# Kernel optimization log

Hardware: AMD Instinct MI355X
Metric: run time of the kernel (lower is better)

## Reference

```python
import jax, jax.numpy as jnp
import numpy as np

N_HEAD, D_MODEL, D_K, D_V = 8, 512, 64, 64
WINDOW, THRESH = 2, 0.5
TEMP = float(np.sqrt(D_K))
LN_EPS = 1e-5


def setup_inputs() -> dict:
    key = jax.random.key(0)
    ks = jax.random.split(key, 12)
    B, L = 4, 2048
    std_qk = np.sqrt(2.0 / (D_MODEL + D_K))
    std_v = np.sqrt(2.0 / (D_MODEL + D_V))
    return {
        "q": jax.random.normal(ks[0], (B, L, D_MODEL), jnp.float32),
        "k": jax.random.normal(ks[1], (B, L, D_MODEL), jnp.float32),
        "v": jax.random.normal(ks[2], (B, L, D_MODEL), jnp.float32),
        "w_q": jax.random.normal(ks[3], (N_HEAD * D_K, D_MODEL), jnp.float32) * std_qk,
        "b_q": jnp.zeros((N_HEAD * D_K,), jnp.float32),
        "w_k": jax.random.normal(ks[4], (N_HEAD * D_K, D_MODEL), jnp.float32) * std_qk,
        "b_k": jnp.zeros((N_HEAD * D_K,), jnp.float32),
        "w_v": jax.random.normal(ks[5], (N_HEAD * D_V, D_MODEL), jnp.float32) * std_v,
        "b_v": jnp.zeros((N_HEAD * D_V,), jnp.float32),
        "w_g": jax.random.normal(ks[6], (1, D_K), jnp.float32) * (1.0 / np.sqrt(D_K)),
        "b_g": jnp.zeros((1,), jnp.float32),
        "w_fc": jax.random.normal(ks[7], (D_MODEL, N_HEAD * D_V), jnp.float32) * (1.0 / np.sqrt(D_MODEL)),
        "b_fc": jnp.zeros((D_MODEL,), jnp.float32),
        "ln_g": jnp.ones((D_MODEL,), jnp.float32),
        "ln_b": jnp.zeros((D_MODEL,), jnp.float32),
    }


def reference(q, k, v, w_q, b_q, w_k, b_k, w_v, b_v, w_g, b_g, w_fc, b_fc, ln_g, ln_b):
    B, Lq, _ = q.shape
    Lk = k.shape[1]
    residual = q
    # project and split heads: (h, B, L, d)
    qh = (q @ w_q.T + b_q).reshape(B, Lq, N_HEAD, D_K).transpose(2, 0, 1, 3)
    kh = (k @ w_k.T + b_k).reshape(B, Lk, N_HEAD, D_K).transpose(2, 0, 1, 3)
    vh = (v @ w_v.T + b_v).reshape(B, Lk, N_HEAD, D_V).transpose(2, 0, 1, 3)

    scores = jnp.einsum('hbqd,hbkd->hbqk', qh, kh) / TEMP  # (h, B, Lq, Lk)

    # dynamic gate: tokens with sigmoid(gate) > THRESH keep full attention,
    # others are restricted to a +/-WINDOW sliding window
    gate_open = jax.nn.sigmoid(jnp.einsum('hbqd,od->hbqo', qh, w_g) + b_g)[..., 0] > THRESH
    i = jnp.arange(Lq)[:, None]
    j = jnp.arange(Lk)[None, :]
    win = jnp.abs(i - j) <= WINDOW  # (Lq, Lk)
    allowed = gate_open[..., None] | win  # (h, B, Lq, Lk)
    scores = jnp.where(allowed, scores, -jnp.inf)

    attn = jax.nn.softmax(scores, axis=-1)  # dropout is identity in eval
    out = jnp.einsum('hbqk,hbkd->hbqd', attn, vh)
    out = out.transpose(1, 2, 0, 3).reshape(B, Lq, N_HEAD * D_V)
    out = out @ w_fc.T + b_fc

    x = out + residual
    mu = jnp.mean(x, axis=-1, keepdims=True)
    var = jnp.mean((x - mu) ** 2, axis=-1, keepdims=True)
    out = (x - mu) * jax.lax.rsqrt(var + LN_EPS) * ln_g + ln_b

    return out, attn.reshape(N_HEAD * B, Lq, Lk)
```

## Files before the change

### kernel.cpp

```cpp
#include <hip/hip_runtime.h>


typedef _Float16 f16;
typedef _Float16 f16x8 __attribute__((ext_vector_type(8)));
typedef _Float16 f16x4 __attribute__((ext_vector_type(4)));
typedef float f32x4 __attribute__((ext_vector_type(4)));

#define OUT0_ELEMS (4 * 2048 * 512)

__device__ __forceinline__ f16x8 cvt8(float4 a, float4 b) {
  f16x8 r;
  r[0] = (f16)a.x; r[1] = (f16)a.y; r[2] = (f16)a.z; r[3] = (f16)a.w;
  r[4] = (f16)b.x; r[5] = (f16)b.y; r[6] = (f16)b.z; r[7] = (f16)b.w;
  return r;
}

__global__ __launch_bounds__(256) void prep_kernel(
    const float* __restrict__ w_q, const float* __restrict__ b_q,
    const float* __restrict__ w_g, const float* __restrict__ b_g,
    double* __restrict__ wge, double* __restrict__ bqg) {
  int idx = blockIdx.x * 256 + threadIdx.x;
  if (idx < 4096) {
    int h = idx >> 9, c = idx & 511;
    double acc = 0.0;
    for (int d = 0; d < 64; ++d)
      acc += (double)w_g[d] * (double)w_q[(h * 64 + d) * 512 + c];
    wge[idx] = acc;
  }
  if (idx < 8) {
    double acc = (double)b_g[0];
    for (int d = 0; d < 64; ++d)
      acc += (double)b_q[idx * 64 + d] * (double)w_g[d];
    bqg[idx] = acc;
  }
}

__global__ __launch_bounds__(256) void gate_kernel(
    const float* __restrict__ q, const double* __restrict__ wge,
    const double* __restrict__ bqg, int* __restrict__ gate) {
  int lane = threadIdx.x & 63, wid = threadIdx.x >> 6;
  int tok = blockIdx.x * 4 + wid;
  int b = tok >> 11, l = tok & 2047;
  const float* qr = q + (long)tok * 512;
  float qv[8];
#pragma unroll
  for (int j = 0; j < 8; ++j) qv[j] = qr[lane + 64 * j];
#pragma unroll
  for (int h = 0; h < 8; ++h) {
    double acc = 0.0;
#pragma unroll
    for (int j = 0; j < 8; ++j) acc += (double)qv[j] * wge[h * 512 + lane + 64 * j];
#pragma unroll
    for (int off = 1; off < 64; off <<= 1) acc += __shfl_xor(acc, off);
    double logit = acc + bqg[h];
    if (lane == 0) gate[(h * 4 + b) * 2048 + l] = (logit > 0.0) ? 1 : 0;
  }
}

__global__ __launch_bounds__(256) void compact_kernel(
    const int* __restrict__ gate, unsigned short* __restrict__ perm,
    int* __restrict__ nopen) {
  __shared__ int wsum[4];
  const int hb = blockIdx.x, t = threadIdx.x;
  const int lane = t & 63, wid = t >> 6;
  const int base = hb * 2048;
  int g[8];
  int cnt = 0;
#pragma unroll
  for (int i = 0; i < 8; ++i) { g[i] = gate[base + t * 8 + i]; cnt += g[i]; }
  int inc = cnt;
#pragma unroll
  for (int off = 1; off < 64; off <<= 1) {
    int y = __shfl_up(inc, off);
    if (lane >= off) inc += y;
  }
  if (lane == 63) wsum[wid] = inc;
  __syncthreads();
  int wbase = 0;
  for (int w = 0; w < wid; ++w) wbase += wsum[w];
  const int totOpen = wsum[0] + wsum[1] + wsum[2] + wsum[3];
  int openPos = wbase + inc - cnt;
  int closedPos = totOpen + t * 8 - openPos;
#pragma unroll
  for (int i = 0; i < 8; ++i) {
    int l = t * 8 + i;
    if (g[i]) perm[base + openPos++] = (unsigned short)l;
    else      perm[base + closedPos++] = (unsigned short)l;
  }
  if (t == 0) nopen[hb] = totOpen;
}

template <int EPI>
__global__ __launch_bounds__(256) void gemm512(
    const float* __restrict__ A, const float* __restrict__ W,
    const float* __restrict__ bias, const float* __restrict__ res,
    f16* __restrict__ out16, float* __restrict__ outf) {
  __shared__ __align__(16) f16 As[64 * 32];
  __shared__ __align__(16) f16 Ws[64 * 32];
  const int tid = threadIdx.x;
  const int lane = tid & 63, wid = tid >> 6;
  const int lo = lane & 15, hi = lane >> 4;
  const int m0 = blockIdx.x * 64, n0 = blockIdx.y * 64;
  const int wm = wid >> 1, wn = wid & 1;

  const int srow = tid >> 2, sseg = tid & 3;
  const int ssu = sseg ^ (srow & 3);
  const float* gA = A + (long)(m0 + srow) * 512 + sseg * 8;
  const float* gW = W + (long)(n0 + srow) * 512 + sseg * 8;
  f16* wA = &As[srow * 32 + ssu * 8];
  f16* wW = &Ws[srow * 32 + ssu * 8];

  const f32x4 zero4 = {0.f, 0.f, 0.f, 0.f};
  f32x4 acc[2][2] = {{zero4, zero4}, {zero4, zero4}};
  const int ra0 = wm * 32 + lo;
  const int rb0 = wn * 32 + lo;
  const int sa = hi ^ (ra0 & 3);
  const int sb = hi ^ (rb0 & 3);

  for (int kk = 0; kk < 512; kk += 32) {
    float4 a0 = *(const float4*)(gA + kk);
    float4 a1 = *(const float4*)(gA + kk + 4);
    float4 w0 = *(const float4*)(gW + kk);
    float4 w1 = *(const float4*)(gW + kk + 4);
    *(f16x8*)wA = cvt8(a0, a1);
    *(f16x8*)wW = cvt8(w0, w1);
    __syncthreads();
    f16x8 af0 = *(const f16x8*)&As[ra0 * 32 + sa * 8];
    f16x8 af1 = *(const f16x8*)&As[(ra0 + 16) * 32 + sa * 8];
    f16x8 bf0 = *(const f16x8*)&Ws[rb0 * 32 + sb * 8];
    f16x8 bf1 = *(const f16x8*)&Ws[(rb0 + 16) * 32 + sb * 8];
    acc[0][0] = __builtin_amdgcn_mfma_f32_16x16x32_f16(af0, bf0, acc[0][0], 0, 0, 0);
    acc[0][1] = __builtin_amdgcn_mfma_f32_16x16x32_f16(af0, bf1, acc[0][1], 0, 0, 0);
    acc[1][0] = __builtin_amdgcn_mfma_f32_16x16x32_f16(af1, bf0, acc[1][0], 0, 0, 0);
    acc[1][1] = __builtin_amdgcn_mfma_f32_16x16x32_f16(af1, bf1, acc[1][1], 0, 0, 0);
    __syncthreads();
  }

#pragma unroll
  for (int i = 0; i < 2; ++i)
#pragma unroll
    for (int j = 0; j < 2; ++j)
#pragma unroll
      for (int r = 0; r < 4; ++r) {
        const int m = m0 + wm * 32 + i * 16 + hi * 4 + r;
        const int n = n0 + wn * 32 + j * 16 + lo;
        float v = acc[i][j][r] + bias[n];
        if constexpr (EPI == 0) {
          const int b = m >> 11, l = m & 2047, h = n >> 6, d = n & 63;
          out16[(long)((h * 4 + b) * 2048 + l) * 64 + d] = (f16)v;
        } else if constexpr (EPI == 2) {
          const int b = m >> 11, l = m & 2047, h = n >> 6, d = n & 63;
          out16[(long)((h * 4 + b) * 64 + d) * 2048 + l] = (f16)v;
        } else {
          outf[(long)m * 512 + n] = v + res[(long)m * 512 + n];
        }
      }
}

struct Stg2 { uint4 d0, d1; };

__device__ __forceinline__ Stg2 ldK(const f16* __restrict__ g, int tid) {
  Stg2 s;
  s.d0 = *(const uint4*)(g + tid * 8);
  s.d1 = *(const uint4*)(g + 2048 + tid * 8);
  return s;
}

__device__ __forceinline__ Stg2 ldV(const f16* __restrict__ g, int tid) {
  const int row = tid >> 3, seg = tid & 7;
  const f16* p = g + (long)row * 2048 + seg * 8;
  Stg2 s;
  s.d0 = *(const uint4*)p;
  s.d1 = *(const uint4*)(p + 32 * 2048);
  return s;
}

__device__ __forceinline__ void stW(const Stg2& s, f16* lds, int tid) {
  const int row = tid >> 3, seg = tid & 7, sw = row & 7;
  *(uint4*)&lds[(row << 6) + ((seg ^ sw) << 3)] = s.d0;
  *(uint4*)&lds[((row + 32) << 6) + ((seg ^ sw) << 3)] = s.d1;
}

__global__ __launch_bounds__(256) void attn_kernel(
    const f16* __restrict__ qh, const f16* __restrict__ kh,
    const f16* __restrict__ vt, const int* __restrict__ gate,
    const unsigned short* __restrict__ perm, const int* __restrict__ nopen,
    float* __restrict__ attn, float* __restrict__ o) {
  __shared__ __align__(16) f16 Ks[2][4096];
  __shared__ __align__(16) f16 Vs[2][4096];
  __shared__ __align__(16) f16 Ps[4][1024];
  const int tid = threadIdx.x;
  const int lane = tid & 63, wid = tid >> 6;
  const int bid = blockIdx.x;

  if (bid >= 1024) {
    const int vb = bid - 1024;
    const int hb = vb >> 5, chunk = vb & 31;
    const int nop = nopen[hb];
    const int j0 = ((nop + 63) & ~63) + (chunk << 6);
    if (j0 >= 2048) return;
    unsigned short* rowIdx = (unsigned short*)&Ks[0][0];
    if (tid < 64) rowIdx[tid] = perm[hb * 2048 + j0 + tid];
    __syncthreads();
    float* abase = attn + ((long)hb * 2048 << 11);
    const f32x4 zero4 = {0.f, 0.f, 0.f, 0.f};
#pragma unroll 4
    for (int it = 0; it < 128; ++it) {
      const int c = tid + (it << 8);
      const int ri = c >> 9;
      const int col = (c & 511) << 2;
      *(f32x4*)(abase + ((long)rowIdx[ri] << 11) + col) = zero4;
    }
    __syncthreads();
    const f16* qhb = qh + (long)hb * 2048 * 64;
    const f16* khb = kh + (long)hb * 2048 * 64;
    const f16* vtb = vt + (long)hb * 64 * 2048;
    const int b = hb & 3, h = hb >> 2;
    for (int rr = 0; rr < 16; ++rr) {
      const int row = rowIdx[(wid << 4) + rr];
      const int jlo = max(row - 2, 0), jhi = min(row + 2, 2047);
      const float qv = (float)qhb[(long)row * 64 + lane];
      float p0, p1, p2, p3, p4, sum = 0.f;
#pragma unroll
      for (int jj = 0; jj < 5; ++jj) {
        const int j = jlo + jj;
        const int js = min(j, 2047);
        float prod = qv * (float)khb[(long)js * 64 + lane];
        prod += __shfl_xor(prod, 1);
        prod += __shfl_xor(prod, 2);
        prod += __shfl_xor(prod, 4);
        prod += __shfl_xor(prod, 8);
        prod += __shfl_xor(prod, 16);
        prod += __shfl_xor(prod, 32);
        const float e = (j <= jhi) ? __expf(prod * 0.125f) : 0.f;
        if (jj == 0) p0 = e; else if (jj == 1) p1 = e; else if (jj == 2) p2 = e;
        else if (jj == 3) p3 = e; else p4 = e;
        sum += e;
      }
      const float inv = 1.f / sum;
      float pv = p0;
      pv = (lane == 1) ? p1 : pv;
      pv = (lane == 2) ? p2 : pv;
      pv = (lane == 3) ? p3 : pv;
      pv = (lane == 4) ? p4 : pv;
      if (lane < 5 && (jlo + lane) <= jhi)
        abase[((long)row << 11) + jlo + lane] = pv * inv;
      float od = 0.f;
      od += p0 * (float)vtb[(long)lane * 2048 + min(jlo + 0, 2047)];
      od += p1 * (float)vtb[(long)lane * 2048 + min(jlo + 1, 2047)];
      od += p2 * (float)vtb[(long)lane * 2048 + min(jlo + 2, 2047)];
      od += p3 * (float)vtb[(long)lane * 2048 + min(jlo + 3, 2047)];
      od += p4 * (float)vtb[(long)lane * 2048 + min(jlo + 4, 2047)];
      o[(long)(b * 2048 + row) * 512 + (h << 6) + lane] = od * inv;
    }
    return;
  }

  const int lo = lane & 15, hi = lane >> 4;
  const int xcd = bid & 7, local = bid >> 3;
  const int hb = xcd * 4 + (local >> 5);
  const int q0 = (local & 31) << 6;
  const int nop = nopen[hb];
  if (q0 >= nop) return;

  const unsigned short* pm = perm + hb * 2048 + q0;
  const f16* khb = kh + (long)hb * 2048 * 64;
  const f16* vtb = vt + (long)hb * 64 * 2048;

  const int rowA = pm[(wid << 4) + lo];
  const f16* qrow = qh + (long)(hb * 2048 + rowA) * 64;
  const f16x8 aq0 = *(const f16x8*)(qrow + (hi << 3));
  const f16x8 aq1 = *(const f16x8*)(qrow + 32 + (hi << 3));

  int qi[4], gt[4];
  float psum[4];
#pragma unroll
  for (int r = 0; r < 4; ++r) {
    qi[r] = pm[(wid << 4) + (hi << 2) + r];
    gt[r] = gate[hb * 2048 + qi[r]];
    psum[r] = 0.f;
  }
  const f32x4 zero4 = {0.f, 0.f, 0.f, 0.f};

  {
    Stg2 kreg = ldK(khb, tid);
    stW(kreg, &Ks[0][0], tid);
    kreg = ldK(khb + 4096, tid);
    int cur = 0;
    for (int kt = 0; kt < 32; ++kt) {
      __syncthreads();
      if (kt < 31) {
        stW(kreg, &Ks[cur ^ 1][0], tid);
        if (kt < 30) kreg = ldK(khb + (long)(kt + 2) * 4096, tid);
      }
      const f16* Kc = &Ks[cur][0];
      f32x4 sacc[4] = {zero4, zero4, zero4, zero4};
      __builtin_amdgcn_s_setprio(1);
#pragma unroll
      for (int s = 0; s < 2; ++s) {
        const f16x8 a = s ? aq1 : aq0;
#pragma unroll
        for (int nt = 0; nt < 4; ++nt) {
          const int krow = (nt << 4) + lo;
          const f16x8 b = *(const f16x8*)&Kc[(krow << 6) + ((((s << 2) + hi) ^ (krow & 7)) << 3)];
          sacc[nt] = __builtin_amdgcn_mfma_f32_16x16x32_f16(a, b, sacc[nt], 0, 0, 0);
        }
      }
      __builtin_amdgcn_s_setprio(0);
      const int kkb = (kt << 6) + lo;
#pragma unroll
      for (int nt = 0; nt < 4; ++nt) {
        const int kk = kkb + (nt << 4);
#pragma unroll
        for (int r = 0; r < 4; ++r) {
          const bool allowed = gt[r] || ((unsigned)(kk - qi[r] + 2) <= 4u);
          psum[r] += allowed ? __expf(sacc[nt][r] * 0.125f) : 0.f;
        }
      }
      cur ^= 1;
    }
  }

  float invl[4];
#pragma unroll
  for (int r = 0; r < 4; ++r) {
    float s = psum[r];
    s += __shfl_xor(s, 1);
    s += __shfl_xor(s, 2);
    s += __shfl_xor(s, 4);
    s += __shfl_xor(s, 8);
    invl[r] = 1.f / s;
  }

  f32x4 oacc[4] = {zero4, zero4, zero4, zero4};
  f16* Pw = &Ps[wid][0];
  const int row2 = lane >> 2, qq = lane & 3;
  float* arow = attn + ((long)(hb * 2048 + pm[(wid << 4) + row2]) << 11);

  {
    Stg2 kreg = ldK(khb, tid);
    Stg2 vreg = ldV(vtb, tid);
    stW(kreg, &Ks[0][0], tid);
    stW(vreg, &Vs[0][0], tid);
    kreg = ldK(khb + 4096, tid);
    vreg = ldV(vtb + 64, tid);
    int cur = 0;
    for (int kt = 0; kt < 32; ++kt) {
      __syncthreads();
      if (kt < 31) {
        stW(kreg, &Ks[cur ^ 1][0], tid);
        stW(vreg, &Vs[cur ^ 1][0], tid);
        if (kt < 30) {
          kreg = ldK(khb + (long)(kt + 2) * 4096, tid);
          vreg = ldV(vtb + ((kt + 2) << 6), tid);
        }
      }
      const f16* Kc = &Ks[cur][0];
      const f16* Vc = &Vs[cur][0];
      f32x4 sacc[4] = {zero4, zero4, zero4, zero4};
      __builtin_amdgcn_s_setprio(1);
#pragma unroll
      for (int s = 0; s < 2; ++s) {
        const f16x8 a = s ? aq1 : aq0;
#pragma unroll
        for (int nt = 0; nt < 4; ++nt) {
          const int krow = (nt << 4) + lo;
          const f16x8 b = *(const f16x8*)&Kc[(krow << 6) + ((((s << 2) + hi) ^ (krow & 7)) << 3)];
          sacc[nt] = __builtin_amdgcn_mfma_f32_16x16x32_f16(a, b, sacc[nt], 0, 0, 0);
        }
      }
      __builtin_amdgcn_s_setprio(0);
      const int kkb = (kt << 6) + lo;
#pragma unroll
      for (int nt = 0; nt < 4; ++nt) {
        const int kk = kkb + (nt << 4);
#pragma unroll
        for (int r = 0; r < 4; ++r) {
          const bool allowed = gt[r] || ((unsigned)(kk - qi[r] + 2) <= 4u);
          const float p = allowed ? __expf(sacc[nt][r] * 0.125f) * invl[r] : 0.f;
          const int prow = (hi << 2) + r;
          const int pcol = (nt << 4) + lo;
          Pw[(prow << 6) + (((pcol >> 3) ^ (prow & 7)) << 3) + (pcol & 7)] = (f16)p;
        }
      }
      __builtin_amdgcn_s_setprio(1);
#pragma unroll
      for (int s = 0; s < 2; ++s) {
        const f16x8 ap = *(const f16x8*)&Pw[(lo << 6) + ((((s << 2) + hi) ^ (lo & 7)) << 3)];
#pragma unroll
        for (int nt = 0; nt < 4; ++nt) {
          const int vrow = (nt << 4) + lo;
          const f16x8 bv = *(const f16x8*)&Vc[(vrow << 6) + ((((s << 2) + hi) ^ (vrow & 7)) << 3)];
          oacc[nt] = __builtin_amdgcn_mfma_f32_16x16x32_f16(ap, bv, oacc[nt], 0, 0, 0);
        }
      }
      __builtin_amdgcn_s_setprio(0);
      {
        const int swz = row2 & 7;
        float* dst = arow + (kt << 6) + (qq << 2);
#pragma unroll
        for (int i = 0; i < 4; ++i) {
          const f16x4 pv = *(const f16x4*)&Pw[(row2 << 6) + ((((i << 1) + (qq >> 1)) ^ swz) << 3) + ((qq & 1) << 2)];
          f32x4 fo = {(float)pv[0], (float)pv[1], (float)pv[2], (float)pv[3]};
          *(f32x4*)(dst + (i << 4)) = fo;
        }
      }
      cur ^= 1;
    }
  }

  const int b = hb & 3, h = hb >> 2;
#pragma unroll
  for (int nt = 0; nt < 4; ++nt)
#pragma unroll
    for (int r = 0; r < 4; ++r)
      o[(long)(b * 2048 + qi[r]) * 512 + (h << 6) + (nt << 4) + lo] = oacc[nt][r];
}

__global__ __launch_bounds__(256) void ln_kernel(float* __restrict__ x,
                                                 const float* __restrict__ g,
                                                 const float* __restrict__ bta) {
  __shared__ float red[8];
  const int t = threadIdx.x;
  float* row = x + (long)blockIdx.x * 512;
  float v0 = row[t], v1 = row[t + 256];
  float s = v0 + v1;
#pragma unroll
  for (int off = 1; off < 64; off <<= 1) s += __shfl_xor(s, off);
  if ((t & 63) == 0) red[t >> 6] = s;
  __syncthreads();
  const float mean = (red[0] + red[1] + red[2] + red[3]) * (1.f / 512.f);
  const float d0 = v0 - mean, d1 = v1 - mean;
  float sq = d0 * d0 + d1 * d1;
#pragma unroll
  for (int off = 1; off < 64; off <<= 1) sq += __shfl_xor(sq, off);
  if ((t & 63) == 0) red[4 + (t >> 6)] = sq;
  __syncthreads();
  const float var = (red[4] + red[5] + red[6] + red[7]) * (1.f / 512.f);
  const float rstd = 1.f / sqrtf(var + 1e-5f);
  row[t] = d0 * rstd * g[t] + bta[t];
  row[t + 256] = d1 * rstd * g[t + 256] + bta[t + 256];
}

extern "C" void kernel_launch(void* const* d_in, const int* in_sizes, int n_in,
                              void* d_out, int out_size, void* d_ws, size_t ws_size,
                              hipStream_t stream) {
  const float* q    = (const float*)d_in[0];
  const float* k    = (const float*)d_in[1];
  const float* v    = (const float*)d_in[2];
  const float* w_q  = (const float*)d_in[3];
  const float* b_q  = (const float*)d_in[4];
  const float* w_k  = (const float*)d_in[5];
  const float* b_k  = (const float*)d_in[6];
  const float* w_v  = (const float*)d_in[7];
  const float* b_v  = (const float*)d_in[8];
  const float* w_g  = (const float*)d_in[9];
  const float* b_g  = (const float*)d_in[10];
  const float* w_fc = (const float*)d_in[11];
  const float* b_fc = (const float*)d_in[12];
  const float* ln_g = (const float*)d_in[13];
  const float* ln_b = (const float*)d_in[14];

  char* wsb = (char*)d_ws;
  f16* qh16   = (f16*)wsb;
  f16* kh16   = qh16 + 4194304;
  f16* vt16   = kh16 + 4194304;
  float* ob   = (float*)(wsb + 25165824);
  int* gateb  = (int*)(wsb + 25165824 + 16777216);
  double* wge = (double*)(wsb + 25165824 + 16777216 + 262144);
  double* bqg = wge + 4096;
  unsigned short* permb = (unsigned short*)(wsb + 25165824 + 16777216 + 262144 + 32768 + 64);
  int* nopenb = (int*)(wsb + 25165824 + 16777216 + 262144 + 32768 + 64 + 131072);

  float* out0 = (float*)d_out;
  float* attn = out0 + OUT0_ELEMS;

  prep_kernel<<<16, 256, 0, stream>>>(w_q, b_q, w_g, b_g, wge, bqg);
  gate_kernel<<<2048, 256, 0, stream>>>(q, wge, bqg, gateb);
  compact_kernel<<<32, 256, 0, stream>>>(gateb, permb, nopenb);

  dim3 gp(128, 8);
  gemm512<0><<<gp, 256, 0, stream>>>(q, w_q, b_q, nullptr, qh16, nullptr);
  gemm512<0><<<gp, 256, 0, stream>>>(k, w_k, b_k, nullptr, kh16, nullptr);
  gemm512<2><<<gp, 256, 0, stream>>>(v, w_v, b_v, nullptr, vt16, nullptr);

  attn_kernel<<<2048, 256, 0, stream>>>(qh16, kh16, vt16, gateb, permb, nopenb, attn, ob);

  gemm512<3><<<gp, 256, 0, stream>>>(ob, w_fc, b_fc, q, nullptr, out0);
  ln_kernel<<<8192, 256, 0, stream>>>(out0, ln_g, ln_b);
}
```

Measured before the change: 314.5 us.

## Use 512-thread attention blocks over 128 query rows to halve K/V staging

Attention blocks grow from 256 to 512 threads (8 waves), and each block handles 128 gathered query rows instead of 64. Each K/V tile staged in LDS is therefore shared by twice as many rows, which halves global K/V traffic per query, and each thread now loads one 16-byte chunk instead of two. Barriers become an explicit LDS waitcnt plus s_barrier rather than __syncthreads, and the window-only blocks are remapped by XCD with 128-aligned starts. The trade-off is fewer blocks and possibly lower occupancy from larger blocks and doubled P scratch, plus more wasted rows when a head's open count is not a multiple of 128.

```diff
diff --git a/kernel.cpp b/kernel.cpp
--- a/kernel.cpp
+++ b/kernel.cpp
@@ -13,6 +13,11 @@
   r[0] = (f16)a.x; r[1] = (f16)a.y; r[2] = (f16)a.z; r[3] = (f16)a.w;
   r[4] = (f16)b.x; r[5] = (f16)b.y; r[6] = (f16)b.z; r[7] = (f16)b.w;
   return r;
+}
+
+__device__ __forceinline__ void bar_lds() {
+  asm volatile("s_waitcnt lgkmcnt(0)" ::: "memory");
+  __builtin_amdgcn_s_barrier();
 }
 
 __global__ __launch_bounds__(256) void prep_kernel(
@@ -157,67 +162,51 @@
       }
 }
 
-struct Stg2 { uint4 d0, d1; };
-
-__device__ __forceinline__ Stg2 ldK(const f16* __restrict__ g, int tid) {
-  Stg2 s;
-  s.d0 = *(const uint4*)(g + tid * 8);
-  s.d1 = *(const uint4*)(g + 2048 + tid * 8);
-  return s;
-}
-
-__device__ __forceinline__ Stg2 ldV(const f16* __restrict__ g, int tid) {
-  const int row = tid >> 3, seg = tid & 7;
-  const f16* p = g + (long)row * 2048 + seg * 8;
-  Stg2 s;
-  s.d0 = *(const uint4*)p;
-  s.d1 = *(const uint4*)(p + 32 * 2048);
-  return s;
-}
-
-__device__ __forceinline__ void stW(const Stg2& s, f16* lds, int tid) {
+__device__ __forceinline__ uint4 ldK512(const f16* __restrict__ g, int tid) {
+  return *(const uint4*)(g + tid * 8);
+}
+__device__ __forceinline__ uint4 ldV512(const f16* __restrict__ g, int tid) {
+  return *(const uint4*)(g + (long)(tid >> 3) * 2048 + ((tid & 7) << 3));
+}
+__device__ __forceinline__ void stW512(uint4 s, f16* lds, int tid) {
   const int row = tid >> 3, seg = tid & 7, sw = row & 7;
-  *(uint4*)&lds[(row << 6) + ((seg ^ sw) << 3)] = s.d0;
-  *(uint4*)&lds[((row + 32) << 6) + ((seg ^ sw) << 3)] = s.d1;
-}
-
-__global__ __launch_bounds__(256) void attn_kernel(
+  *(uint4*)&lds[(row << 6) + ((seg ^ sw) << 3)] = s;
+}
+
+__global__ __launch_bounds__(512) void attn_kernel(
     const f16* __restrict__ qh, const f16* __restrict__ kh,
     const f16* __restrict__ vt, const int* __restrict__ gate,
     const unsigned short* __restrict__ perm, const int* __restrict__ nopen,
     float* __restrict__ attn, float* __restrict__ o) {
   __shared__ __align__(16) f16 Ks[2][4096];
   __shared__ __align__(16) f16 Vs[2][4096];
-  __shared__ __align__(16) f16 Ps[4][1024];
+  __shared__ __align__(16) f16 Ps[8][1024];
   const int tid = threadIdx.x;
   const int lane = tid & 63, wid = tid >> 6;
   const int bid = blockIdx.x;
 
-  if (bid >= 1024) {
-    const int vb = bid - 1024;
-    const int hb = vb >> 5, chunk = vb & 31;
+  if (bid >= 512) {
+    const int vb = bid - 512;
+    const int xcd = vb & 7, sub = vb >> 3;
+    const int hb = xcd * 4 + (sub >> 5);
+    const int chunk = sub & 31;
     const int nop = nopen[hb];
-    const int j0 = ((nop + 63) & ~63) + (chunk << 6);
+    const int j0 = ((nop + 127) & ~127) + (chunk << 6);
     if (j0 >= 2048) return;
     unsigned short* rowIdx = (unsigned short*)&Ks[0][0];
     if (tid < 64) rowIdx[tid] = perm[hb * 2048 + j0 + tid];
     __syncthreads();
     float* abase = attn + ((long)hb * 2048 << 11);
     const f32x4 zero4 = {0.f, 0.f, 0.f, 0.f};
-#pragma unroll 4
-    for (int it = 0; it < 128; ++it) {
-      const int c = tid + (it << 8);
-      const int ri = c >> 9;
-      const int col = (c & 511) << 2;
-      *(f32x4*)(abase + ((long)rowIdx[ri] << 11) + col) = zero4;
-    }
+    for (int it = 0; it < 64; ++it)
+      *(f32x4*)(abase + ((long)rowIdx[it] << 11) + (tid << 2)) = zero4;
     __syncthreads();
     const f16* qhb = qh + (long)hb * 2048 * 64;
     const f16* khb = kh + (long)hb * 2048 * 64;
     const f16* vtb = vt + (long)hb * 64 * 2048;
     const int b = hb & 3, h = hb >> 2;
-    for (int rr = 0; rr < 16; ++rr) {
-      const int row = rowIdx[(wid << 4) + rr];
+    for (int rr = 0; rr < 8; ++rr) {
+      const int row = rowIdx[(wid << 3) + rr];
       const int jlo = max(row - 2, 0), jhi = min(row + 2, 2047);
       const float qv = (float)qhb[(long)row * 64 + lane];
       float p0, p1, p2, p3, p4, sum = 0.f;
@@ -258,8 +247,8 @@
 
   const int lo = lane & 15, hi = lane >> 4;
   const int xcd = bid & 7, local = bid >> 3;
-  const int hb = xcd * 4 + (local >> 5);
-  const int q0 = (local & 31) << 6;
+  const int hb = xcd * 4 + (local >> 4);
+  const int q0 = (local & 15) << 7;
   const int nop = nopen[hb];
   if (q0 >= nop) return;
 
@@ -283,15 +272,15 @@
   const f32x4 zero4 = {0.f, 0.f, 0.f, 0.f};
 
   {
-    Stg2 kreg = ldK(khb, tid);
-    stW(kreg, &Ks[0][0], tid);
-    kreg = ldK(khb + 4096, tid);
+    uint4 kreg = ldK512(khb, tid);
+    stW512(kreg, &Ks[0][0], tid);
+    kreg = ldK512(khb + 4096, tid);
     int cur = 0;
     for (int kt = 0; kt < 32; ++kt) {
-      __syncthreads();
+      bar_lds();
       if (kt < 31) {
-        stW(kreg, &Ks[cur ^ 1][0], tid);
-        if (kt < 30) kreg = ldK(khb + (long)(kt + 2) * 4096, tid);
+        stW512(kreg, &Ks[cur ^ 1][0], tid);
+        if (kt < 30) kreg = ldK512(khb + (long)(kt + 2) * 4096, tid);
       }
       const f16* Kc = &Ks[cur][0];
       f32x4 sacc[4] = {zero4, zero4, zero4, zero4};
@@ -338,21 +327,21 @@
   float* arow = attn + ((long)(hb * 2048 + pm[(wid << 4) + row2]) << 11);
 
   {
-    Stg2 kreg = ldK(khb, tid);
-    Stg2 vreg = ldV(vtb, tid);
-    stW(kreg, &Ks[0][0], tid);
-    stW(vreg, &Vs[0][0], tid);
-    kreg = ldK(khb + 4096, tid);
-    vreg = ldV(vtb + 64, tid);
+    uint4 kreg = ldK512(khb, tid);
+    uint4 vreg = ldV512(vtb, tid);
+    stW512(kreg, &Ks[0][0], tid);
+    stW512(vreg, &Vs[0][0], tid);
+    kreg = ldK512(khb + 4096, tid);
+    vreg = ldV512(vtb + 64, tid);
     int cur = 0;
     for (int kt = 0; kt < 32; ++kt) {
-      __syncthreads();
+      bar_lds();
       if (kt < 31) {
-        stW(kreg, &Ks[cur ^ 1][0], tid);
-        stW(vreg, &Vs[cur ^ 1][0], tid);
+        stW512(kreg, &Ks[cur ^ 1][0], tid);
+        stW512(vreg, &Vs[cur ^ 1][0], tid);
         if (kt < 30) {
-          kreg = ldK(khb + (long)(kt + 2) * 4096, tid);
-          vreg = ldV(vtb + ((kt + 2) << 6), tid);
+          kreg = ldK512(khb + (long)(kt + 2) * 4096, tid);
+          vreg = ldV512(vtb + ((kt + 2) << 6), tid);
         }
       }
       const f16* Kc = &Ks[cur][0];
@@ -484,7 +473,7 @@
   gemm512<0><<<gp, 256, 0, stream>>>(k, w_k, b_k, nullptr, kh16, nullptr);
   gemm512<2><<<gp, 256, 0, stream>>>(v, w_v, b_v, nullptr, vt16, nullptr);
 
-  attn_kernel<<<2048, 256, 0, stream>>>(qh16, kh16, vt16, gateb, permb, nopenb, attn, ob);
+  attn_kernel<<<1536, 512, 0, stream>>>(qh16, kh16, vt16, gateb, permb, nopenb, attn, ob);
 
   gemm512<3><<<gp, 256, 0, stream>>>(ob, w_fc, b_fc, q, nullptr, out0);
   ln_kernel<<<8192, 256, 0, stream>>>(out0, ln_g, ln_b);
```

Measured after the change: 269.6 us. 14.3% less time.
